# Performance work log

Hardware: AMD Instinct MI355X
Metric: run time of the kernel (lower is better)

The kernel has to match this reference:

```python
import jax, jax.numpy as jnp
import numpy as np

D = 512; N = 4096; NH = 16; DEPTH = 3; MLP = 4; GENES = 250; GH = 64; GW = 64


def setup_inputs() -> dict:
    key = jax.random.key(0)
    ks = jax.random.split(key, 10)
    gf = jax.random.normal(ks[0], (N, D), jnp.float32)
    # unique spot positions: permutation of the 64x64 grid cells
    perm = jax.random.permutation(ks[1], GH * GW)[:N]
    coords = jnp.stack([perm // GW, perm % GW], axis=1).astype(jnp.int32)
    s = 0.02
    rn = lambda k, sh: jax.random.normal(k, sh, jnp.float32) * s
    return dict(
        global_feats=gf, coords=coords, grid_h=GH, grid_w=GW,
        ln1_g=jnp.ones((DEPTH, D)), ln1_b=jnp.zeros((DEPTH, D)),
        wqkv=rn(ks[2], (DEPTH, 3 * D, D)), bqkv=jnp.zeros((DEPTH, 3 * D)),
        wo=rn(ks[3], (DEPTH, D, D)), bo=jnp.zeros((DEPTH, D)),
        ln2_g=jnp.ones((DEPTH, D)), ln2_b=jnp.zeros((DEPTH, D)),
        w1=rn(ks[4], (DEPTH, MLP * D, D)), b1=jnp.zeros((DEPTH, MLP * D)),
        w2=rn(ks[5], (DEPTH, D, MLP * D)), b2=jnp.zeros((DEPTH, D)),
        ck=rn(ks[6], (DEPTH, D, 1, 3, 3)), cb=jnp.zeros((DEPTH, D)),
        lnf_g=jnp.ones((D,)), lnf_b=jnp.zeros((D,)),
        wp=rn(ks[7], (GENES, D)), bp=jnp.zeros((GENES,)),
    )


def _ln(x, g, b, eps=1e-5):
    m = jnp.mean(x, axis=-1, keepdims=True)
    v = jnp.var(x, axis=-1, keepdims=True)
    return (x - m) * jax.lax.rsqrt(v + eps) * g + b


def reference(global_feats, coords, grid_h, grid_w, ln1_g, ln1_b, wqkv, bqkv,
              wo, bo, ln2_g, ln2_b, w1, b1, w2, b2, ck, cb, lnf_g, lnf_b, wp, bp):
    x = global_feats  # [N, D]
    n, d = x.shape
    nh = NH; dh = d // nh
    rows = coords[:, 0]; cols = coords[:, 1]
    for i in range(ln1_g.shape[0]):
        # --- self-attention (eval mode, dropout off) ---
        xn = _ln(x, ln1_g[i], ln1_b[i])
        qkv = xn @ wqkv[i].T + bqkv[i]                      # [N, 3D]
        q, k, v = jnp.split(qkv, 3, axis=-1)
        q = q.reshape(n, nh, dh).transpose(1, 0, 2)        # [H, N, dh]
        k = k.reshape(n, nh, dh).transpose(1, 0, 2)
        v = v.reshape(n, nh, dh).transpose(1, 0, 2)
        att = jax.nn.softmax(jnp.einsum('hqd,hkd->hqk', q, k) * (dh ** -0.5), axis=-1)
        ao = jnp.einsum('hqk,hkd->hqd', att, v).transpose(1, 0, 2).reshape(n, d)
        x = x + (ao @ wo[i].T + bo[i])
        # --- MLP ---
        h = jax.nn.gelu(_ln(x, ln2_g[i], ln2_b[i]) @ w1[i].T + b1[i], approximate=False)
        x = x + (h @ w2[i].T + b2[i])
        # --- APEG: scatter -> depthwise conv -> gather ---
        grid = jnp.zeros((d, grid_h, grid_w), x.dtype).at[:, rows, cols].set(x.T)
        co = jax.lax.conv_general_dilated(
            grid[None], ck[i], window_strides=(1, 1), padding=((1, 1), (1, 1)),
            dimension_numbers=('NCHW', 'OIHW', 'NCHW'), feature_group_count=d)[0]
        co = co + cb[i][:, None, None]
        x = x + co[:, rows, cols].T
    x = _ln(x, lnf_g, lnf_b)
    pred = x @ wp.T + bp
    return (x, pred)
```

## Files before the change

### kernel.cpp

```cpp
#include <hip/hip_runtime.h>
#include <math.h>

#define D 512
#define N_TOK 4096
#define NHEAD 16
#define DH 32
#define DEPTH 3
#define MLPD 2048
#define GENES 250
#define GH 64
#define GW 64

typedef __attribute__((ext_vector_type(8))) short short8;
typedef __attribute__((ext_vector_type(4))) float f32x4;
typedef unsigned short ushort_t;

#define AS1 __attribute__((address_space(1)))
#define AS3 __attribute__((address_space(3)))

#if defined(__has_builtin)
#if __has_builtin(__builtin_amdgcn_exp2f)
#define EXP2F(x) __builtin_amdgcn_exp2f(x)
#endif
#endif
#ifndef EXP2F
#define EXP2F(x) __expf(0.69314718056f * (x))
#endif

__device__ __forceinline__ unsigned short f2bf(float f) {
  unsigned int u = __float_as_uint(f);
  u += 0x7fffu + ((u >> 16) & 1u);
  return (unsigned short)(u >> 16);
}
__device__ __forceinline__ unsigned int bfpack(float a, float b) {
  return __builtin_amdgcn_perm(__float_as_uint(b), __float_as_uint(a), 0x07060302u);
}
__device__ __forceinline__ void gload_lds16(const ushort_t* g, ushort_t* l) {
  __builtin_amdgcn_global_load_lds(
      (const AS1 unsigned int*)g,
      (AS3 unsigned int*)(unsigned int)(unsigned long long)l, 16, 0, 0);
}
__device__ __forceinline__ int perm64(int m) {
  int mi = m >> 4, g = (m >> 2) & 3, r = m & 3;
  return ((mi & 1) << 5) | (g << 3) | ((mi >> 1) << 2) | r;
}

__global__ __launch_bounds__(256) void ln_kernel(const float* __restrict__ x,
    const float* __restrict__ g, const float* __restrict__ b,
    float* __restrict__ yf, ushort_t* __restrict__ ybf) {
  int row = blockIdx.x;
  int t = threadIdx.x;
  const float* xr = x + (size_t)row * D;
  float v0 = xr[t], v1 = xr[t + 256];
  float s = v0 + v1;
  float sq = v0 * v0 + v1 * v1;
#pragma unroll
  for (int off = 32; off > 0; off >>= 1) {
    s += __shfl_down(s, off, 64);
    sq += __shfl_down(sq, off, 64);
  }
  __shared__ float s1[4], s2[4];
  int wid = t >> 6, lane = t & 63;
  if (lane == 0) { s1[wid] = s; s2[wid] = sq; }
  __syncthreads();
  float tot = s1[0] + s1[1] + s1[2] + s1[3];
  float totq = s2[0] + s2[1] + s2[2] + s2[3];
  float mean = tot * (1.0f / D);
  float var = totq * (1.0f / D) - mean * mean;
  float rs = rsqrtf(var + 1e-5f);
  float r0 = (v0 - mean) * rs * g[t] + b[t];
  float r1 = (v1 - mean) * rs * g[t + 256] + b[t + 256];
  if (yf) { yf[(size_t)row * D + t] = r0; yf[(size_t)row * D + t + 256] = r1; }
  if (ybf) {
    ybf[(size_t)row * D + t] = f2bf(r0);
    ybf[(size_t)row * D + t + 256] = f2bf(r1);
  }
}

template <int TM, int TN, int NKH>
__global__ __launch_bounds__(256) void gemm_bf(
    const ushort_t* __restrict__ A, const ushort_t* __restrict__ B,
    const float* __restrict__ bias, const float* __restrict__ res,
    float* __restrict__ C, ushort_t* __restrict__ Cbf,
    ushort_t* __restrict__ qO, ushort_t* __restrict__ kO, ushort_t* __restrict__ vO,
    int K, int ldc, int nstore, int mode) {
  constexpr int MI = TM / 32;
  constexpr int NI = TN / 32;
  __shared__ ushort_t As[2][NKH][TM * 32];
  __shared__ ushort_t Bs[2][NKH][TN * 32];
  int t = threadIdx.x;
  int w = t >> 6, lane = t & 63;
  int g = lane >> 4, c = lane & 15;
  int bm = blockIdx.y * TM, bn = blockIdx.x * TN;
  int wr = (w >> 1) * (TM / 2);
  int wc = (w & 1) * (TN / 2);

  const ushort_t* gA = A + (size_t)(bm + (t >> 2)) * K + (t & 3) * 8;
  const ushort_t* gB = B + (size_t)(bn + (t >> 2)) * K + (t & 3) * 8;

  auto stage = [&](int p, int koff) {
#pragma unroll
    for (int h = 0; h < NKH; ++h) {
      gload_lds16(gA + koff + h * 32, &As[p][h][t * 8]);
      if (TM == 128)
        gload_lds16(gA + koff + h * 32 + (size_t)64 * K, &As[p][h][(t + 256) * 8]);
      gload_lds16(gB + koff + h * 32, &Bs[p][h][t * 8]);
      if (TN == 128)
        gload_lds16(gB + koff + h * 32 + (size_t)64 * K, &Bs[p][h][(t + 256) * 8]);
    }
  };

  f32x4 acc[MI][NI] = {};

  const int niter = K / (32 * NKH);
  stage(0, 0);
  __syncthreads();
  for (int it = 0; it < niter; ++it) {
    int p = it & 1;
    if (it + 1 < niter) stage(p ^ 1, (it + 1) * 32 * NKH);
#pragma unroll
    for (int kh = 0; kh < NKH; ++kh) {
      short8 af[MI], bfr[NI];
#pragma unroll
      for (int mi = 0; mi < MI; ++mi)
        af[mi] = *(const short8*)&As[p][kh][(wr + mi * 16 + c) * 32 + g * 8];
#pragma unroll
      for (int ni = 0; ni < NI; ++ni)
        bfr[ni] = *(const short8*)&Bs[p][kh][(wc + ni * 16 + c) * 32 + g * 8];
#pragma unroll
      for (int mi = 0; mi < MI; ++mi)
#pragma unroll
        for (int ni = 0; ni < NI; ++ni)
          acc[mi][ni] = __builtin_amdgcn_mfma_f32_16x16x32_bf16(
              af[mi], bfr[ni], acc[mi][ni], 0, 0, 0);
    }
    __syncthreads();
  }

  const float qs_scale = 0.17677669529663688f * 1.4426950408889634f;
  if (mode == 2) {
#pragma unroll
    for (int ni = 0; ni < NI; ++ni) {
      int col = bn + wc + ni * 16 + c;
      float bv = bias[col];
      int which = col >> 9;
      int h = (col >> 5) & 15;
      int d = col & 31;
      size_t hb = (size_t)h * (N_TOK * DH);
#pragma unroll
      for (int mi = 0; mi < MI; ++mi) {
        int row0 = bm + wr + mi * 16 + g * 4;
        float v0 = acc[mi][ni][0] + bv;
        float v1 = acc[mi][ni][1] + bv;
        float v2 = acc[mi][ni][2] + bv;
        float v3 = acc[mi][ni][3] + bv;
        if (which == 0) {
          qO[hb + (size_t)(row0 + 0) * DH + d] = f2bf(v0 * qs_scale);
          qO[hb + (size_t)(row0 + 1) * DH + d] = f2bf(v1 * qs_scale);
          qO[hb + (size_t)(row0 + 2) * DH + d] = f2bf(v2 * qs_scale);
          qO[hb + (size_t)(row0 + 3) * DH + d] = f2bf(v3 * qs_scale);
        } else if (which == 1) {
          kO[hb + (size_t)(row0 + 0) * DH + d] = f2bf(v0);
          kO[hb + (size_t)(row0 + 1) * DH + d] = f2bf(v1);
          kO[hb + (size_t)(row0 + 2) * DH + d] = f2bf(v2);
          kO[hb + (size_t)(row0 + 3) * DH + d] = f2bf(v3);
        } else {
          int m = row0 & 63;
          int mi_l = m >> 4, g_l = (m >> 2) & 3;
          int nb = ((mi_l & 1) << 5) | (g_l << 3) | ((mi_l >> 1) << 2);
          uint2 pk;
          pk.x = (unsigned)f2bf(v0) | ((unsigned)f2bf(v1) << 16);
          pk.y = (unsigned)f2bf(v2) | ((unsigned)f2bf(v3) << 16);
          *(uint2*)(vO + hb + (size_t)d * N_TOK + (row0 & ~63) + nb) = pk;
        }
      }
    }
    return;
  }
#pragma unroll
  for (int ni = 0; ni < NI; ++ni) {
    int col = bn + wc + ni * 16 + c;
    float bv = bias[col];
    bool cok = col < nstore;
#pragma unroll
    for (int mi = 0; mi < MI; ++mi) {
      int row0 = bm + wr + mi * 16 + g * 4;
#pragma unroll
      for (int reg = 0; reg < 4; ++reg) {
        int row = row0 + reg;
        float v = acc[mi][ni][reg] + bv;
        if (mode == 0) {
          size_t idx = (size_t)row * ldc + col;
          if (cok) {
            if (res) v += res[idx];
            C[idx] = v;
          }
        } else {
          v = 0.5f * v * (1.0f + erff(v * 0.70710678118654752f));
          Cbf[(size_t)row * ldc + col] = f2bf(v);
        }
      }
    }
  }
}

#define KST 40
#define VTST 72

__global__ __launch_bounds__(256) void attn_mfma(
    const ushort_t* __restrict__ qb, const ushort_t* __restrict__ kb,
    const ushort_t* __restrict__ vtb, ushort_t* __restrict__ ao) {
  __shared__ ushort_t Ks[64 * KST];
  __shared__ ushort_t Vts[32 * VTST];
  int qt = blockIdx.x, head = blockIdx.y;
  int t = threadIdx.x;
  int w = t >> 6, lane = t & 63;
  int g = lane >> 4, c = lane & 15;
  const size_t hbase = (size_t)head * (N_TOK * DH);
  int q0 = qt * 128 + w * 32;

  short8 qf[2];
  qf[0] = *(const short8*)(qb + hbase + (size_t)(q0 + c) * DH + g * 8);
  qf[1] = *(const short8*)(qb + hbase + (size_t)(q0 + 16 + c) * DH + g * 8);

  short8 ones;
#pragma unroll
  for (int i = 0; i < 8; ++i) ones[i] = (short)0x3F80;

  f32x4 o[2][2] = {};
  f32x4 lf[2] = {};
  const f32x4 zf = {0.f, 0.f, 0.f, 0.f};

  const ushort_t* kg = kb + hbase + (size_t)(t >> 2) * DH + (t & 3) * 8;
  const ushort_t* vg = vtb + hbase + (size_t)(t >> 3) * N_TOK + (t & 7) * 8;
  ushort_t* kw = &Ks[(t >> 2) * KST + (t & 3) * 8];
  ushort_t* vw = &Vts[(t >> 3) * VTST + (t & 7) * 8];

  short8 kreg = *(const short8*)kg;
  short8 vreg = *(const short8*)vg;

  typedef union { short8 s8; unsigned int u32[4]; } pk_t;

  for (int tile = 0; tile < N_TOK / 64; ++tile) {
    __syncthreads();
    *(short8*)kw = kreg;
    *(short8*)vw = vreg;
    __syncthreads();
    if (tile + 1 < N_TOK / 64) {
      kreg = *(const short8*)(kg + (size_t)(tile + 1) * 64 * DH);
      vreg = *(const short8*)(vg + (tile + 1) * 64);
    }

    short8 kf[4];
#pragma unroll
    for (int mi = 0; mi < 4; ++mi)
      kf[mi] = *(const short8*)&Ks[(mi * 16 + c) * KST + g * 8];
    short8 vf[2][2];
#pragma unroll
    for (int half = 0; half < 2; ++half)
#pragma unroll
      for (int ch = 0; ch < 2; ++ch)
        vf[half][ch] = *(const short8*)&Vts[(half * 16 + c) * VTST + ch * 32 + g * 8];

    short8 pf[2][2];
#pragma unroll
    for (int qs = 0; qs < 2; ++qs) {
      f32x4 sp[4];
#pragma unroll
      for (int mi = 0; mi < 4; ++mi)
        sp[mi] = __builtin_amdgcn_mfma_f32_16x16x32_bf16(kf[mi], qf[qs], zf, 0, 0, 0);
      float pr[4][4];
#pragma unroll
      for (int mi = 0; mi < 4; ++mi)
#pragma unroll
        for (int r = 0; r < 4; ++r) pr[mi][r] = EXP2F(sp[mi][r]);
      pk_t p0, p1;
      p0.u32[0] = bfpack(pr[0][0], pr[0][1]);
      p0.u32[1] = bfpack(pr[0][2], pr[0][3]);
      p0.u32[2] = bfpack(pr[2][0], pr[2][1]);
      p0.u32[3] = bfpack(pr[2][2], pr[2][3]);
      p1.u32[0] = bfpack(pr[1][0], pr[1][1]);
      p1.u32[1] = bfpack(pr[1][2], pr[1][3]);
      p1.u32[2] = bfpack(pr[3][0], pr[3][1]);
      p1.u32[3] = bfpack(pr[3][2], pr[3][3]);
      pf[qs][0] = p0.s8;
      pf[qs][1] = p1.s8;
    }

#pragma unroll
    for (int qs = 0; qs < 2; ++qs) {
#pragma unroll
      for (int ch = 0; ch < 2; ++ch) {
        lf[qs] = __builtin_amdgcn_mfma_f32_16x16x32_bf16(ones, pf[qs][ch], lf[qs], 0, 0, 0);
#pragma unroll
        for (int half = 0; half < 2; ++half)
          o[qs][half] = __builtin_amdgcn_mfma_f32_16x16x32_bf16(
              vf[half][ch], pf[qs][ch], o[qs][half], 0, 0, 0);
      }
    }
  }

#pragma unroll
  for (int qs = 0; qs < 2; ++qs) {
    float inv = 1.0f / lf[qs][0];
    int q = q0 + qs * 16 + c;
    ushort_t* op = ao + (size_t)q * D + head * DH;
#pragma unroll
    for (int half = 0; half < 2; ++half)
#pragma unroll
      for (int reg = 0; reg < 4; ++reg)
        op[half * 16 + g * 4 + reg] = f2bf(o[qs][half][reg] * inv);
  }
}

__global__ void scatter_kernel(const int* __restrict__ coords,
                               int* __restrict__ pos2tok) {
  int n = blockIdx.x * 256 + threadIdx.x;
  if (n < N_TOK) pos2tok[coords[2 * n] * GW + coords[2 * n + 1]] = n;
}

__global__ __launch_bounds__(256) void conv_ln_kernel(
    const float* __restrict__ xin, float* __restrict__ xout,
    const float* __restrict__ ck, const float* __restrict__ cb,
    const int* __restrict__ pos2tok, const int* __restrict__ coords,
    const float* __restrict__ g, const float* __restrict__ b,
    float* __restrict__ yf, ushort_t* __restrict__ ybf) {
  int n = blockIdx.x, t = threadIdx.x;
  __shared__ int nb[9];
  if (t < 9) {
    int r = coords[2 * n], c = coords[2 * n + 1];
    int dy = t / 3 - 1, dx = t % 3 - 1;
    int rr = r + dy, cc = c + dx;
    nb[t] = (rr >= 0 && rr < GH && cc >= 0 && cc < GW) ? pos2tok[rr * GW + cc] : -1;
  }
  __syncthreads();
  float v[2];
#pragma unroll
  for (int j = 0; j < 2; ++j) {
    int ch = t + j * 256;
    float s = cb[ch];
#pragma unroll
    for (int tap = 0; tap < 9; ++tap) {
      int tok = nb[tap];
      if (tok >= 0) s = fmaf(ck[ch * 9 + tap], xin[(size_t)tok * D + ch], s);
    }
    v[j] = xin[(size_t)n * D + ch] + s;
    xout[(size_t)n * D + ch] = v[j];
  }
  float s = v[0] + v[1];
  float sq = v[0] * v[0] + v[1] * v[1];
#pragma unroll
  for (int off = 32; off > 0; off >>= 1) {
    s += __shfl_down(s, off, 64);
    sq += __shfl_down(sq, off, 64);
  }
  __shared__ float s1[4], s2[4];
  int wid = t >> 6, lane = t & 63;
  if (lane == 0) { s1[wid] = s; s2[wid] = sq; }
  __syncthreads();
  float tot = s1[0] + s1[1] + s1[2] + s1[3];
  float totq = s2[0] + s2[1] + s2[2] + s2[3];
  float mean = tot * (1.0f / D);
  float var = totq * (1.0f / D) - mean * mean;
  float rs = rsqrtf(var + 1e-5f);
  float r0 = (v[0] - mean) * rs * g[t] + b[t];
  float r1 = (v[1] - mean) * rs * g[t + 256] + b[t + 256];
  if (yf) { yf[(size_t)n * D + t] = r0; yf[(size_t)n * D + t + 256] = r1; }
  ybf[(size_t)n * D + t] = f2bf(r0);
  ybf[(size_t)n * D + t + 256] = f2bf(r1);
}

__global__ __launch_bounds__(256) void castw(const float* __restrict__ src,
    ushort_t* __restrict__ dst, int n_src, int n_dst) {
  int i = (blockIdx.x * 256 + threadIdx.x) * 4;
  if (i >= n_dst) return;
  unsigned long long pk = 0;
#pragma unroll
  for (int j = 0; j < 4; ++j) {
    float v = (i + j < n_src) ? src[i + j] : 0.f;
    pk |= ((unsigned long long)f2bf(v)) << (16 * j);
  }
  *(unsigned long long*)(dst + i) = pk;
}

__global__ void pad_bias(const float* __restrict__ src, float* __restrict__ dst) {
  int i = threadIdx.x;
  dst[i] = (i < GENES) ? src[i] : 0.f;
}

extern "C" void kernel_launch(void* const* d_in, const int* in_sizes, int n_in,
                              void* d_out, int out_size, void* d_ws, size_t ws_size,
                              hipStream_t stream) {
  const float* gf     = (const float*)d_in[0];
  const int*   coords = (const int*)d_in[1];
  const float* ln1_g  = (const float*)d_in[4];
  const float* ln1_b  = (const float*)d_in[5];
  const float* wqkv   = (const float*)d_in[6];
  const float* bqkv   = (const float*)d_in[7];
  const float* wo     = (const float*)d_in[8];
  const float* bo     = (const float*)d_in[9];
  const float* ln2_g  = (const float*)d_in[10];
  const float* ln2_b  = (const float*)d_in[11];
  const float* w1     = (const float*)d_in[12];
  const float* b1     = (const float*)d_in[13];
  const float* w2     = (const float*)d_in[14];
  const float* b2     = (const float*)d_in[15];
  const float* ck     = (const float*)d_in[16];
  const float* cb     = (const float*)d_in[17];
  const float* lnf_g  = (const float*)d_in[18];
  const float* lnf_b  = (const float*)d_in[19];
  const float* wp     = (const float*)d_in[20];
  const float* bp     = (const float*)d_in[21];
  float* out = (float*)d_out;

  const size_t ND = (size_t)N_TOK * D;
  float* xb0 = (float*)d_ws;
  float* xb1 = xb0 + ND;
  ushort_t* xn_bf  = (ushort_t*)(xb1 + ND);
  ushort_t* ao_bf  = xn_bf + ND;
  ushort_t* out_bf = ao_bf + ND;
  ushort_t* shared = out_bf + ND;
  ushort_t* qb   = shared;
  ushort_t* kbuf = qb + ND;
  ushort_t* vtb  = kbuf + ND;
  ushort_t* h_bf = shared;
  ushort_t* wqkv_bf = shared + (size_t)N_TOK * MLPD;
  ushort_t* wo_bf = wqkv_bf + DEPTH * 3 * D * D;
  ushort_t* w1_bf = wo_bf + DEPTH * D * D;
  ushort_t* w2_bf = w1_bf + DEPTH * MLPD * D;
  ushort_t* wp_bf = w2_bf + DEPTH * D * MLPD;
  float* bp_pad = (float*)(wp_bf + 256 * D);
  int* pos2tok = (int*)(bp_pad + 256);

  hipMemcpyAsync(xb0, gf, ND * sizeof(float), hipMemcpyDeviceToDevice, stream);
  hipMemsetAsync(pos2tok, 0xFF, GH * GW * sizeof(int), stream);
  scatter_kernel<<<(N_TOK + 255) / 256, 256, 0, stream>>>(coords, pos2tok);

  int nw;
  nw = DEPTH * 3 * D * D;  castw<<<(nw / 4 + 255) / 256, 256, 0, stream>>>(wqkv, wqkv_bf, nw, nw);
  nw = DEPTH * D * D;      castw<<<(nw / 4 + 255) / 256, 256, 0, stream>>>(wo, wo_bf, nw, nw);
  nw = DEPTH * MLPD * D;   castw<<<(nw / 4 + 255) / 256, 256, 0, stream>>>(w1, w1_bf, nw, nw);
  nw = DEPTH * D * MLPD;   castw<<<(nw / 4 + 255) / 256, 256, 0, stream>>>(w2, w2_bf, nw, nw);
  castw<<<(256 * D / 4 + 255) / 256, 256, 0, stream>>>(wp, wp_bf, GENES * D, 256 * D);
  pad_bias<<<1, 256, 0, stream>>>(bp, bp_pad);

  ln_kernel<<<N_TOK, 256, 0, stream>>>(xb0, ln1_g, ln1_b, nullptr, xn_bf);

  float* x  = xb0;
  float* xo = xb1;
  for (int i = 0; i < DEPTH; ++i) {
    gemm_bf<128, 128, 1><<<dim3(12, 32), 256, 0, stream>>>(
        xn_bf, wqkv_bf + (size_t)i * 3 * D * D, bqkv + (size_t)i * 3 * D,
        nullptr, nullptr, nullptr, qb, kbuf, vtb, D, 0, 3 * D, 2);
    attn_mfma<<<dim3(N_TOK / 128, NHEAD), 256, 0, stream>>>(qb, kbuf, vtb, ao_bf);
    gemm_bf<64, 64, 2><<<dim3(8, 64), 256, 0, stream>>>(
        ao_bf, wo_bf + (size_t)i * D * D, bo + (size_t)i * D,
        x, x, nullptr, nullptr, nullptr, nullptr, D, D, D, 0);
    ln_kernel<<<N_TOK, 256, 0, stream>>>(x, ln2_g + i * D, ln2_b + i * D, nullptr, xn_bf);
    gemm_bf<128, 128, 1><<<dim3(16, 32), 256, 0, stream>>>(
        xn_bf, w1_bf + (size_t)i * MLPD * D, b1 + (size_t)i * MLPD,
        nullptr, nullptr, h_bf, nullptr, nullptr, nullptr, D, MLPD, MLPD, 1);
    gemm_bf<64, 64, 2><<<dim3(8, 64), 256, 0, stream>>>(
        h_bf, w2_bf + (size_t)i * D * MLPD, b2 + (size_t)i * D,
        x, x, nullptr, nullptr, nullptr, nullptr, MLPD, D, D, 0);
    if (i < DEPTH - 1) {
      conv_ln_kernel<<<N_TOK, 256, 0, stream>>>(
          x, xo, ck + (size_t)i * D * 9, cb + (size_t)i * D, pos2tok, coords,
          ln1_g + (i + 1) * D, ln1_b + (i + 1) * D, nullptr, xn_bf);
    } else {
      conv_ln_kernel<<<N_TOK, 256, 0, stream>>>(
          x, xo, ck + (size_t)i * D * 9, cb + (size_t)i * D, pos2tok, coords,
          lnf_g, lnf_b, out, out_bf);
    }
    float* tmp = x; x = xo; xo = tmp;
  }
  gemm_bf<64, 64, 2><<<dim3(4, 64), 256, 0, stream>>>(
      out_bf, wp_bf, bp_pad, nullptr, out + ND, nullptr, nullptr, nullptr, nullptr,
      D, GENES, GENES, 0);
}
```

Baseline: 624.2 us.

## Add split-K atomics, triple-buffered GEMM pipeline, and double-buffered attention K/V tiles

The GEMM main loop moves to a three-stage LDS ring with explicit vmcnt waits and one raw barrier per step, so global loads run two tiles ahead of compute. The Wo, W2 and final projection GEMMs now split K across blockIdx.z and accumulate into the output with float atomicAdd; the residual is picked up by accumulating directly into x, and the prediction buffer is zeroed beforehand. Attention double-buffers its K/V shared-memory tiles, which drops one barrier per tile. The atomics make accumulation order nondeterministic and add atomic traffic, in exchange for more blocks on the narrow GEMMs.

After: 701.6 us. 1.12x slower.

```diff
diff --git a/kernel.cpp b/kernel.cpp
--- a/kernel.cpp
+++ b/kernel.cpp
@@ -39,6 +39,12 @@
   __builtin_amdgcn_global_load_lds(
       (const AS1 unsigned int*)g,
       (AS3 unsigned int*)(unsigned int)(unsigned long long)l, 16, 0, 0);
+}
+template <int N>
+__device__ __forceinline__ void wait_vm_lgkm0() {
+  if constexpr (N == 0) __builtin_amdgcn_s_waitcnt(0x070);
+  else if constexpr (N == 2) __builtin_amdgcn_s_waitcnt(0x072);
+  else __builtin_amdgcn_s_waitcnt(0x074);
 }
 __device__ __forceinline__ int perm64(int m) {
   int mi = m >> 4, g = (m >> 2) & 3, r = m & 3;
@@ -77,64 +83,61 @@
   }
 }
 
-template <int TM, int TN, int NKH>
+template <int TM, int TN>
 __global__ __launch_bounds__(256) void gemm_bf(
     const ushort_t* __restrict__ A, const ushort_t* __restrict__ B,
-    const float* __restrict__ bias, const float* __restrict__ res,
+    const float* __restrict__ bias,
     float* __restrict__ C, ushort_t* __restrict__ Cbf,
     ushort_t* __restrict__ qO, ushort_t* __restrict__ kO, ushort_t* __restrict__ vO,
-    int K, int ldc, int nstore, int mode) {
+    int K, int lda, int ldc, int nstore, int mode) {
   constexpr int MI = TM / 32;
   constexpr int NI = TN / 32;
-  __shared__ ushort_t As[2][NKH][TM * 32];
-  __shared__ ushort_t Bs[2][NKH][TN * 32];
+  constexpr int LD = (TM == 128 ? 2 : 1) + (TN == 128 ? 2 : 1);
+  __shared__ ushort_t As[3][TM * 32];
+  __shared__ ushort_t Bs[3][TN * 32];
   int t = threadIdx.x;
   int w = t >> 6, lane = t & 63;
   int g = lane >> 4, c = lane & 15;
   int bm = blockIdx.y * TM, bn = blockIdx.x * TN;
+  int kbase = blockIdx.z * K;
   int wr = (w >> 1) * (TM / 2);
   int wc = (w & 1) * (TN / 2);
 
-  const ushort_t* gA = A + (size_t)(bm + (t >> 2)) * K + (t & 3) * 8;
-  const ushort_t* gB = B + (size_t)(bn + (t >> 2)) * K + (t & 3) * 8;
-
-  auto stage = [&](int p, int koff) {
-#pragma unroll
-    for (int h = 0; h < NKH; ++h) {
-      gload_lds16(gA + koff + h * 32, &As[p][h][t * 8]);
-      if (TM == 128)
-        gload_lds16(gA + koff + h * 32 + (size_t)64 * K, &As[p][h][(t + 256) * 8]);
-      gload_lds16(gB + koff + h * 32, &Bs[p][h][t * 8]);
-      if (TN == 128)
-        gload_lds16(gB + koff + h * 32 + (size_t)64 * K, &Bs[p][h][(t + 256) * 8]);
-    }
+  const ushort_t* gA = A + (size_t)(bm + (t >> 2)) * lda + kbase + (t & 3) * 8;
+  const ushort_t* gB = B + (size_t)(bn + (t >> 2)) * lda + kbase + (t & 3) * 8;
+
+  auto stage = [&](int s, int koff) {
+    gload_lds16(gA + koff, &As[s][t * 8]);
+    if (TM == 128) gload_lds16(gA + koff + (size_t)64 * lda, &As[s][(t + 256) * 8]);
+    gload_lds16(gB + koff, &Bs[s][t * 8]);
+    if (TN == 128) gload_lds16(gB + koff + (size_t)64 * lda, &Bs[s][(t + 256) * 8]);
   };
 
   f32x4 acc[MI][NI] = {};
-
-  const int niter = K / (32 * NKH);
+  const int niter = K / 32;
   stage(0, 0);
-  __syncthreads();
+  stage(1, 32);
+  wait_vm_lgkm0<LD>();
+  __builtin_amdgcn_s_barrier();
   for (int it = 0; it < niter; ++it) {
-    int p = it & 1;
-    if (it + 1 < niter) stage(p ^ 1, (it + 1) * 32 * NKH);
-#pragma unroll
-    for (int kh = 0; kh < NKH; ++kh) {
-      short8 af[MI], bfr[NI];
-#pragma unroll
-      for (int mi = 0; mi < MI; ++mi)
-        af[mi] = *(const short8*)&As[p][kh][(wr + mi * 16 + c) * 32 + g * 8];
+    int p = it % 3;
+    if (it + 2 < niter) stage((it + 2) % 3, (it + 2) * 32);
+    short8 af[MI], bfr[NI];
+#pragma unroll
+    for (int mi = 0; mi < MI; ++mi)
+      af[mi] = *(const short8*)&As[p][(wr + mi * 16 + c) * 32 + g * 8];
+#pragma unroll
+    for (int ni = 0; ni < NI; ++ni)
+      bfr[ni] = *(const short8*)&Bs[p][(wc + ni * 16 + c) * 32 + g * 8];
+#pragma unroll
+    for (int mi = 0; mi < MI; ++mi)
 #pragma unroll
       for (int ni = 0; ni < NI; ++ni)
-        bfr[ni] = *(const short8*)&Bs[p][kh][(wc + ni * 16 + c) * 32 + g * 8];
-#pragma unroll
-      for (int mi = 0; mi < MI; ++mi)
-#pragma unroll
-        for (int ni = 0; ni < NI; ++ni)
-          acc[mi][ni] = __builtin_amdgcn_mfma_f32_16x16x32_bf16(
-              af[mi], bfr[ni], acc[mi][ni], 0, 0, 0);
-    }
-    __syncthreads();
+        acc[mi][ni] = __builtin_amdgcn_mfma_f32_16x16x32_bf16(
+            af[mi], bfr[ni], acc[mi][ni], 0, 0, 0);
+    if (it + 2 < niter) wait_vm_lgkm0<LD>();
+    else wait_vm_lgkm0<0>();
+    __builtin_amdgcn_s_barrier();
   }
 
   const float qs_scale = 0.17677669529663688f * 1.4426950408889634f;
@@ -177,6 +180,7 @@
     }
     return;
   }
+  bool addb = (blockIdx.z == 0);
 #pragma unroll
   for (int ni = 0; ni < NI; ++ni) {
     int col = bn + wc + ni * 16 + c;
@@ -188,14 +192,13 @@
 #pragma unroll
       for (int reg = 0; reg < 4; ++reg) {
         int row = row0 + reg;
-        float v = acc[mi][ni][reg] + bv;
-        if (mode == 0) {
-          size_t idx = (size_t)row * ldc + col;
-          if (cok) {
-            if (res) v += res[idx];
-            C[idx] = v;
-          }
+        float v = acc[mi][ni][reg];
+        if (mode == 3) {
+          if (cok) atomicAdd(&C[(size_t)row * ldc + col], v + (addb ? bv : 0.f));
+        } else if (mode == 0) {
+          if (cok) C[(size_t)row * ldc + col] = v + bv;
         } else {
+          v += bv;
           v = 0.5f * v * (1.0f + erff(v * 0.70710678118654752f));
           Cbf[(size_t)row * ldc + col] = f2bf(v);
         }
@@ -206,12 +209,13 @@
 
 #define KST 40
 #define VTST 72
+#define NTILE (N_TOK / 64)
 
 __global__ __launch_bounds__(256) void attn_mfma(
     const ushort_t* __restrict__ qb, const ushort_t* __restrict__ kb,
     const ushort_t* __restrict__ vtb, ushort_t* __restrict__ ao) {
-  __shared__ ushort_t Ks[64 * KST];
-  __shared__ ushort_t Vts[32 * VTST];
+  __shared__ ushort_t Ks[2][64 * KST];
+  __shared__ ushort_t Vts[2][32 * VTST];
   int qt = blockIdx.x, head = blockIdx.y;
   int t = threadIdx.x;
   int w = t >> 6, lane = t & 63;
@@ -233,34 +237,40 @@
 
   const ushort_t* kg = kb + hbase + (size_t)(t >> 2) * DH + (t & 3) * 8;
   const ushort_t* vg = vtb + hbase + (size_t)(t >> 3) * N_TOK + (t & 7) * 8;
-  ushort_t* kw = &Ks[(t >> 2) * KST + (t & 3) * 8];
-  ushort_t* vw = &Vts[(t >> 3) * VTST + (t & 7) * 8];
+  const int kwo = (t >> 2) * KST + (t & 3) * 8;
+  const int vwo = (t >> 3) * VTST + (t & 7) * 8;
 
   short8 kreg = *(const short8*)kg;
   short8 vreg = *(const short8*)vg;
+  *(short8*)&Ks[0][kwo] = kreg;
+  *(short8*)&Vts[0][vwo] = vreg;
+  kreg = *(const short8*)(kg + (size_t)64 * DH);
+  vreg = *(const short8*)(vg + 64);
+  __syncthreads();
 
   typedef union { short8 s8; unsigned int u32[4]; } pk_t;
 
-  for (int tile = 0; tile < N_TOK / 64; ++tile) {
-    __syncthreads();
-    *(short8*)kw = kreg;
-    *(short8*)vw = vreg;
-    __syncthreads();
-    if (tile + 1 < N_TOK / 64) {
-      kreg = *(const short8*)(kg + (size_t)(tile + 1) * 64 * DH);
-      vreg = *(const short8*)(vg + (tile + 1) * 64);
+  for (int tile = 0; tile < NTILE; ++tile) {
+    int p = tile & 1;
+    if (tile + 1 < NTILE) {
+      *(short8*)&Ks[p ^ 1][kwo] = kreg;
+      *(short8*)&Vts[p ^ 1][vwo] = vreg;
+      if (tile + 2 < NTILE) {
+        kreg = *(const short8*)(kg + (size_t)(tile + 2) * 64 * DH);
+        vreg = *(const short8*)(vg + (tile + 2) * 64);
+      }
     }
 
     short8 kf[4];
 #pragma unroll
     for (int mi = 0; mi < 4; ++mi)
-      kf[mi] = *(const short8*)&Ks[(mi * 16 + c) * KST + g * 8];
+      kf[mi] = *(const short8*)&Ks[p][(mi * 16 + c) * KST + g * 8];
     short8 vf[2][2];
 #pragma unroll
     for (int half = 0; half < 2; ++half)
 #pragma unroll
       for (int ch = 0; ch < 2; ++ch)
-        vf[half][ch] = *(const short8*)&Vts[(half * 16 + c) * VTST + ch * 32 + g * 8];
+        vf[half][ch] = *(const short8*)&Vts[p][(half * 16 + c) * VTST + ch * 32 + g * 8];
 
     short8 pf[2][2];
 #pragma unroll
@@ -298,6 +308,7 @@
               vf[half][ch], pf[qs][ch], o[qs][half], 0, 0, 0);
       }
     }
+    __syncthreads();
   }
 
 #pragma unroll
@@ -434,6 +445,7 @@
 
   hipMemcpyAsync(xb0, gf, ND * sizeof(float), hipMemcpyDeviceToDevice, stream);
   hipMemsetAsync(pos2tok, 0xFF, GH * GW * sizeof(int), stream);
+  hipMemsetAsync(out + ND, 0, (size_t)N_TOK * GENES * sizeof(float), stream);
   scatter_kernel<<<(N_TOK + 255) / 256, 256, 0, stream>>>(coords, pos2tok);
 
   int nw;
@@ -449,20 +461,20 @@
   float* x  = xb0;
   float* xo = xb1;
   for (int i = 0; i < DEPTH; ++i) {
-    gemm_bf<128, 128, 1><<<dim3(12, 32), 256, 0, stream>>>(
+    gemm_bf<128, 128><<<dim3(12, 32, 1), 256, 0, stream>>>(
         xn_bf, wqkv_bf + (size_t)i * 3 * D * D, bqkv + (size_t)i * 3 * D,
-        nullptr, nullptr, nullptr, qb, kbuf, vtb, D, 0, 3 * D, 2);
+        nullptr, nullptr, qb, kbuf, vtb, D, D, 0, 3 * D, 2);
     attn_mfma<<<dim3(N_TOK / 128, NHEAD), 256, 0, stream>>>(qb, kbuf, vtb, ao_bf);
-    gemm_bf<64, 64, 2><<<dim3(8, 64), 256, 0, stream>>>(
+    gemm_bf<64, 64><<<dim3(8, 64, 2), 256, 0, stream>>>(
         ao_bf, wo_bf + (size_t)i * D * D, bo + (size_t)i * D,
-        x, x, nullptr, nullptr, nullptr, nullptr, D, D, D, 0);
+        x, nullptr, nullptr, nullptr, nullptr, D / 2, D, D, D, 3);
     ln_kernel<<<N_TOK, 256, 0, stream>>>(x, ln2_g + i * D, ln2_b + i * D, nullptr, xn_bf);
-    gemm_bf<128, 128, 1><<<dim3(16, 32), 256, 0, stream>>>(
+    gemm_bf<128, 128><<<dim3(16, 32, 1), 256, 0, stream>>>(
         xn_bf, w1_bf + (size_t)i * MLPD * D, b1 + (size_t)i * MLPD,
-        nullptr, nullptr, h_bf, nullptr, nullptr, nullptr, D, MLPD, MLPD, 1);
-    gemm_bf<64, 64, 2><<<dim3(8, 64), 256, 0, stream>>>(
+        nullptr, h_bf, nullptr, nullptr, nullptr, D, D, MLPD, MLPD, 1);
+    gemm_bf<64, 64><<<dim3(8, 64, 4), 256, 0, stream>>>(
         h_bf, w2_bf + (size_t)i * D * MLPD, b2 + (size_t)i * D,
-        x, x, nullptr, nullptr, nullptr, nullptr, MLPD, D, D, 0);
+        x, nullptr, nullptr, nullptr, nullptr, MLPD / 4, MLPD, D, D, 3);
     if (i < DEPTH - 1) {
       conv_ln_kernel<<<N_TOK, 256, 0, stream>>>(
           x, xo, ck + (size_t)i * D * 9, cb + (size_t)i * D, pos2tok, coords,
@@ -474,7 +486,7 @@
     }
     float* tmp = x; x = xo; xo = tmp;
   }
-  gemm_bf<64, 64, 2><<<dim3(4, 64), 256, 0, stream>>>(
-      out_bf, wp_bf, bp_pad, nullptr, out + ND, nullptr, nullptr, nullptr, nullptr,
-      D, GENES, GENES, 0);
-}
+  gemm_bf<64, 64><<<dim3(4, 64, 2), 256, 0, stream>>>(
+      out_bf, wp_bf, bp_pad, out + ND, nullptr, nullptr, nullptr, nullptr,
+      D / 2, D, GENES, GENES, 3);
+}
```

## Split attention over two KV halves and merge partial results in a separate kernel

Applied to the files above, without the earlier changes.

The attention kernel gains a third grid dimension that splits the 4096 keys into two halves. Each half writes unnormalized fp32 partial outputs and row sums to a workspace, and a new merge kernel adds them, normalizes, converts to bf16 and transposes back to token-major layout. The aim is to double the number of attention blocks so more of the GPU's compute units stay busy. In exchange it adds extra global-memory traffic for the fp32 partials and one extra kernel launch per layer.

Measured after the change: 633.2 us. No clear change (+1.4%).

```diff
diff --git a/kernel.cpp b/kernel.cpp
--- a/kernel.cpp
+++ b/kernel.cpp
@@ -209,10 +209,11 @@
 
 __global__ __launch_bounds__(256) void attn_mfma(
     const ushort_t* __restrict__ qb, const ushort_t* __restrict__ kb,
-    const ushort_t* __restrict__ vtb, ushort_t* __restrict__ ao) {
+    const ushort_t* __restrict__ vtb, float* __restrict__ po,
+    float* __restrict__ lp) {
   __shared__ ushort_t Ks[64 * KST];
   __shared__ ushort_t Vts[32 * VTST];
-  int qt = blockIdx.x, head = blockIdx.y;
+  int qt = blockIdx.x, head = blockIdx.y, z = blockIdx.z;
   int t = threadIdx.x;
   int w = t >> 6, lane = t & 63;
   int g = lane >> 4, c = lane & 15;
@@ -231,8 +232,9 @@
   f32x4 lf[2] = {};
   const f32x4 zf = {0.f, 0.f, 0.f, 0.f};
 
-  const ushort_t* kg = kb + hbase + (size_t)(t >> 2) * DH + (t & 3) * 8;
-  const ushort_t* vg = vtb + hbase + (size_t)(t >> 3) * N_TOK + (t & 7) * 8;
+  const int kv0 = z * (N_TOK / 2);
+  const ushort_t* kg = kb + hbase + (size_t)(kv0 + (t >> 2)) * DH + (t & 3) * 8;
+  const ushort_t* vg = vtb + hbase + (size_t)(t >> 3) * N_TOK + kv0 + (t & 7) * 8;
   ushort_t* kw = &Ks[(t >> 2) * KST + (t & 3) * 8];
   ushort_t* vw = &Vts[(t >> 3) * VTST + (t & 7) * 8];
 
@@ -241,12 +243,13 @@
 
   typedef union { short8 s8; unsigned int u32[4]; } pk_t;
 
-  for (int tile = 0; tile < N_TOK / 64; ++tile) {
+  const int ntile = N_TOK / 2 / 64;
+  for (int tile = 0; tile < ntile; ++tile) {
     __syncthreads();
     *(short8*)kw = kreg;
     *(short8*)vw = vreg;
     __syncthreads();
-    if (tile + 1 < N_TOK / 64) {
+    if (tile + 1 < ntile) {
       kreg = *(const short8*)(kg + (size_t)(tile + 1) * 64 * DH);
       vreg = *(const short8*)(vg + (tile + 1) * 64);
     }
@@ -302,15 +305,39 @@
 
 #pragma unroll
   for (int qs = 0; qs < 2; ++qs) {
-    float inv = 1.0f / lf[qs][0];
     int q = q0 + qs * 16 + c;
-    ushort_t* op = ao + (size_t)q * D + head * DH;
+    if (g == 0) lp[((size_t)z * NHEAD + head) * N_TOK + q] = lf[qs][0];
 #pragma unroll
     for (int half = 0; half < 2; ++half)
 #pragma unroll
-      for (int reg = 0; reg < 4; ++reg)
-        op[half * 16 + g * 4 + reg] = f2bf(o[qs][half][reg] * inv);
-  }
+      for (int reg = 0; reg < 4; ++reg) {
+        int d = half * 16 + g * 4 + reg;
+        po[(((size_t)z * NHEAD + head) * DH + d) * N_TOK + q] = o[qs][half][reg];
+      }
+  }
+}
+
+__global__ __launch_bounds__(256) void attn_merge(
+    const float* __restrict__ po, const float* __restrict__ lp,
+    ushort_t* __restrict__ ao) {
+  __shared__ ushort_t tile[DH][72];
+  int qt = blockIdx.x, head = blockIdx.y;
+  int t = threadIdx.x;
+  int qBase = qt * 64;
+  int d = t >> 3, qc = (t & 7) * 8;
+  const float* o0 = po + ((size_t)(0 * NHEAD + head) * DH + d) * N_TOK + qBase + qc;
+  const float* o1 = po + ((size_t)(1 * NHEAD + head) * DH + d) * N_TOK + qBase + qc;
+  const float* l0 = lp + (size_t)(0 * NHEAD + head) * N_TOK + qBase + qc;
+  const float* l1 = lp + (size_t)(1 * NHEAD + head) * N_TOK + qBase + qc;
+#pragma unroll
+  for (int j = 0; j < 8; ++j)
+    tile[d][qc + j] = f2bf((o0[j] + o1[j]) / (l0[j] + l1[j]));
+  __syncthreads();
+  int ql = t >> 2, dc = (t & 3) * 8;
+  short8 v;
+#pragma unroll
+  for (int j = 0; j < 8; ++j) v[j] = (short)tile[dc + j][ql];
+  *(short8*)(ao + (size_t)(qBase + ql) * D + head * DH + dc) = v;
 }
 
 __global__ void scatter_kernel(const int* __restrict__ coords,
@@ -431,6 +458,8 @@
   ushort_t* wp_bf = w2_bf + DEPTH * D * MLPD;
   float* bp_pad = (float*)(wp_bf + 256 * D);
   int* pos2tok = (int*)(bp_pad + 256);
+  float* po = (float*)(pos2tok + GH * GW);
+  float* lp = po + (size_t)2 * NHEAD * DH * N_TOK;
 
   hipMemcpyAsync(xb0, gf, ND * sizeof(float), hipMemcpyDeviceToDevice, stream);
   hipMemsetAsync(pos2tok, 0xFF, GH * GW * sizeof(int), stream);
@@ -452,7 +481,8 @@
     gemm_bf<128, 128, 1><<<dim3(12, 32), 256, 0, stream>>>(
         xn_bf, wqkv_bf + (size_t)i * 3 * D * D, bqkv + (size_t)i * 3 * D,
         nullptr, nullptr, nullptr, qb, kbuf, vtb, D, 0, 3 * D, 2);
-    attn_mfma<<<dim3(N_TOK / 128, NHEAD), 256, 0, stream>>>(qb, kbuf, vtb, ao_bf);
+    attn_mfma<<<dim3(N_TOK / 128, NHEAD, 2), 256, 0, stream>>>(qb, kbuf, vtb, po, lp);
+    attn_merge<<<dim3(N_TOK / 64, NHEAD), 256, 0, stream>>>(po, lp, ao_bf);
     gemm_bf<64, 64, 2><<<dim3(8, 64), 256, 0, stream>>>(
         ao_bf, wo_bf + (size_t)i * D * D, bo + (size_t)i * D,
         x, x, nullptr, nullptr, nullptr, nullptr, D, D, D, 0);
```
